# Kernel tuning notes

Hardware: AMD Instinct MI355X
Metric: run time of the kernel (lower is better)

The kernel has to match this reference:

```python
import jax, jax.numpy as jnp
import numpy as np
import math

B, L, D, H = 2, 2048, 1024, 16
DH = D // H
TAU = 1.0
EPS_LN = 1e-12


def neural_sort(scores, tau=TAU):
    # scores: (B, n) -> soft permutation P_hat: (B, n, n)
    s = scores[..., None]                                   # (B,n,1)
    A = jnp.abs(s - jnp.swapaxes(s, 1, 2))                  # (B,n,n) pairwise |s_i - s_j|
    Bsum = jnp.sum(A, axis=-1, keepdims=True)               # row sums == A @ ones(n,n) columns
    n = scores.shape[-1]
    scaling = (n + 1 - 2 * (jnp.arange(n) + 1)).astype(scores.dtype)  # (n,)
    C = s * scaling[None, None, :]                          # (B,n,n)
    P_max = jnp.swapaxes(C - Bsum, 1, 2)
    return jax.nn.softmax(P_max / tau, axis=-1)


def euler_transform(v, delta, b_euler, log_scale, is_query):
    # v: (B,L,D); soft-sort channels, polar decompose, rotate, recompose
    Bv, Lv, Dv = v.shape
    scores = v.mean(axis=1)                                 # (B,D)
    P = neural_sort(scores)                                 # (B,D,D)
    v_sorted = jnp.einsum('bij,blj->bli', P, v)             # permute channel dim
    r, p = v_sorted[..., ::2], v_sorted[..., 1::2]          # (B,L,D/2)
    lam = jnp.sqrt(r * r + p * p + 1e-6)
    lam_d = jax.lax.stop_gradient(lam)
    theta = jnp.arctan2(p / lam_d, r / lam_d)
    theta = theta * delta
    if is_query:
        theta = theta + b_euler
    lam = lam * jnp.exp(jnp.clip(log_scale, -5.0, 5.0))
    out = jnp.stack([lam * jnp.cos(theta), lam * jnp.sin(theta)], axis=-1)
    return out.reshape(Bv, Lv, Dv)


def layer_norm(x, gamma, beta, eps=EPS_LN):
    mu = x.mean(axis=-1, keepdims=True)
    var = ((x - mu) ** 2).mean(axis=-1, keepdims=True)
    return (x - mu) / jnp.sqrt(var + eps) * gamma + beta


def forward(input_tensor, Wq, bq, Wk, bk, Wv, bv, Wd, bd, gamma, beta, delta, b_euler, log_scale):
    q = input_tensor @ Wq.T + bq
    k = input_tensor @ Wk.T + bk
    v = input_tensor @ Wv.T + bv
    q = euler_transform(q, delta, b_euler, log_scale, is_query=True)
    k = euler_transform(k, delta, b_euler, log_scale, is_query=False)
    def heads(x):
        return x.reshape(B, L, H, DH).transpose(0, 2, 1, 3)  # (B,H,L,DH)
    qh, kh, vh = heads(q), heads(k), heads(v)
    scores = jnp.einsum('bhqd,bhkd->bhqk', qh, kh) / math.sqrt(DH)
    probs = jax.nn.softmax(scores, axis=-1)                 # dropout off (eval)
    ctx = jnp.einsum('bhqk,bhkd->bhqd', probs, vh)
    ctx = ctx.transpose(0, 2, 1, 3).reshape(B, L, D)
    hidden = ctx @ Wd.T + bd
    return layer_norm(hidden + input_tensor, gamma, beta)


def setup_inputs() -> dict:
    key = jax.random.key(0)
    ks = jax.random.split(key, 16)
    s = 1.0 / math.sqrt(D)
    return {
        'input_tensor': jax.random.normal(ks[0], (B, L, D), jnp.float32),
        'Wq': jax.random.normal(ks[1], (D, D), jnp.float32) * s,
        'bq': jnp.zeros((D,), jnp.float32),
        'Wk': jax.random.normal(ks[2], (D, D), jnp.float32) * s,
        'bk': jnp.zeros((D,), jnp.float32),
        'Wv': jax.random.normal(ks[3], (D, D), jnp.float32) * s,
        'bv': jnp.zeros((D,), jnp.float32),
        'Wd': jax.random.normal(ks[4], (D, D), jnp.float32) * s,
        'bd': jnp.zeros((D,), jnp.float32),
        'gamma': jnp.ones((D,), jnp.float32),
        'beta': jnp.zeros((D,), jnp.float32),
        'delta': jnp.full((1, 1, D // 2), 0.1, jnp.float32),
        'b_euler': jnp.zeros((1, 1, D // 2), jnp.float32),
        'log_scale': jnp.zeros((1, 1, D // 2), jnp.float32),
    }


def reference(input_tensor, Wq, bq, Wk, bk, Wv, bv, Wd, bd, gamma, beta, delta, b_euler, log_scale):
    return forward(input_tensor, Wq, bq, Wk, bk, Wv, bv, Wd, bd, gamma, beta, delta, b_euler, log_scale)
```

## Files before the change

kernel.cpp:

```cpp
#include <hip/hip_runtime.h>


typedef unsigned short bf16_t;
typedef short frag_ab __attribute__((ext_vector_type(8)));
typedef float frag_cd __attribute__((ext_vector_type(4)));

#define BB 2
#define LL 2048
#define DD 1024
#define HH 16
#define DH 64

__device__ __forceinline__ float b2f(bf16_t u) {
  union { unsigned int i; float f; } c; c.i = ((unsigned int)u) << 16; return c.f;
}
__device__ __forceinline__ bf16_t f2b(float f) {
  union { float f; unsigned int i; } c; c.f = f;
  unsigned int r = c.i + 0x7fffu + ((c.i >> 16) & 1u);
  return (bf16_t)(r >> 16);
}
__device__ __forceinline__ unsigned int fbits(float f) {
  union { float f; unsigned int i; } c; c.f = f; return c.i;
}
__device__ __forceinline__ float waveMax(float v) {
#pragma unroll
  for (int m = 32; m > 0; m >>= 1) v = fmaxf(v, __shfl_xor(v, m));
  return v;
}
__device__ __forceinline__ float waveSum(float v) {
#pragma unroll
  for (int m = 32; m > 0; m >>= 1) v += __shfl_xor(v, m);
  return v;
}

__device__ __forceinline__ void gll16(const bf16_t* g, bf16_t* l) {
  __builtin_amdgcn_global_load_lds(
      (const __attribute__((address_space(1))) void*)g,
      (__attribute__((address_space(3))) void*)l, 16, 0, 0);
}

__global__ __launch_bounds__(256) void cast_f2b(const float* __restrict__ in,
                                                bf16_t* __restrict__ out, int n4) {
  const int i = blockIdx.x * 256 + threadIdx.x;
  if (i < n4) {
    float4 v = ((const float4*)in)[i];
    ushort4 o;
    o.x = f2b(v.x); o.y = f2b(v.y); o.z = f2b(v.z); o.w = f2b(v.w);
    ((ushort4*)out)[i] = o;
  }
}

__global__ __launch_bounds__(256) void cast_wvd(const float* __restrict__ Wv,
                                                const float* __restrict__ Wd,
                                                bf16_t* __restrict__ Wvb,
                                                bf16_t* __restrict__ Wdb) {
  const float* in = blockIdx.z ? Wd : Wv;
  bf16_t* out = blockIdx.z ? Wdb : Wvb;
  const int i = blockIdx.x * 256 + threadIdx.x;
  float4 v = ((const float4*)in)[i];
  ushort4 o;
  o.x = f2b(v.x); o.y = f2b(v.y); o.z = f2b(v.z); o.w = f2b(v.w);
  ((ushort4*)out)[i] = o;
}

__global__ __launch_bounds__(256) void cast_transpose_w(const float* __restrict__ Wq,
                                                        const float* __restrict__ Wk,
                                                        bf16_t* __restrict__ WqT,
                                                        bf16_t* __restrict__ WkT) {
  const float* W = blockIdx.z ? Wk : Wq;
  bf16_t* WT = blockIdx.z ? WkT : WqT;
  __shared__ bf16_t T[64][72];
  const int i0 = blockIdx.x * 64, m0 = blockIdx.y * 64;
  const int tid = threadIdx.x;
#pragma unroll
  for (int it = 0; it < 4; ++it) {
    const int idx = tid + it * 256;
    const int r = idx >> 4, c4 = (idx & 15) * 4;
    float4 v = *(const float4*)&W[(size_t)(i0 + r) * DD + m0 + c4];
    T[c4 + 0][r] = f2b(v.x);
    T[c4 + 1][r] = f2b(v.y);
    T[c4 + 2][r] = f2b(v.z);
    T[c4 + 3][r] = f2b(v.w);
  }
  __syncthreads();
#pragma unroll
  for (int it = 0; it < 2; ++it) {
    const int idx = tid + it * 256;
    const int r = idx >> 3, seg = idx & 7;
    *(uint4*)&WT[(size_t)(m0 + r) * DD + i0 + seg * 8] = *(const uint4*)&T[r][seg * 8];
  }
}

struct GemmB { const bf16_t* A; const bf16_t* Bm; const float* bias; float* Cf; bf16_t* Cb; };
struct GemmArgs { GemmB gb[6]; };

__global__ __launch_bounds__(256) void gemm128(GemmArgs ga, int M, int N, int K) {
  const GemmB g = ga.gb[blockIdx.z];
  const int bm = blockIdx.y * 128, bn = blockIdx.x * 128;
  __shared__ bf16_t As[128][32];
  __shared__ bf16_t Bs[128][32];
  bf16_t* As_f = &As[0][0];
  bf16_t* Bs_f = &Bs[0][0];
  const int tid = threadIdx.x;
  const int lane = tid & 63, w = tid >> 6;
  const int quad = lane >> 4, l16 = lane & 15;
  const int wm = (w >> 1) * 64, wn = (w & 1) * 64;
  const int wbase = w << 9;

  frag_cd acc[4][4];
#pragma unroll
  for (int i = 0; i < 4; ++i)
#pragma unroll
    for (int j = 0; j < 4; ++j)
#pragma unroll
      for (int r = 0; r < 4; ++r) acc[i][j][r] = 0.f;

  const int r0 = tid >> 2, s0 = (tid & 3) * 8;
  const int r1 = (tid + 256) >> 2, s1 = ((tid + 256) & 3) * 8;
  const size_t aoff0 = (size_t)(bm + r0) * K + s0;
  const size_t aoff1 = (size_t)(bm + r1) * K + s1;
  const size_t boff0 = (size_t)(bn + r0) * K + s0;
  const size_t boff1 = (size_t)(bn + r1) * K + s1;

  for (int k0 = 0; k0 < K; k0 += 32) {
    __syncthreads();
    gll16(g.A + aoff0 + k0, As_f + wbase);
    gll16(g.A + aoff1 + k0, As_f + 2048 + wbase);
    gll16(g.Bm + boff0 + k0, Bs_f + wbase);
    gll16(g.Bm + boff1 + k0, Bs_f + 2048 + wbase);
    __syncthreads();
    frag_ab af[4], bfr[4];
#pragma unroll
    for (int i = 0; i < 4; ++i) {
      af[i]  = *(const frag_ab*)&As[wm + i * 16 + l16][quad * 8];
      bfr[i] = *(const frag_ab*)&Bs[wn + i * 16 + l16][quad * 8];
    }
#pragma unroll
    for (int i = 0; i < 4; ++i)
#pragma unroll
      for (int j = 0; j < 4; ++j)
        acc[i][j] = __builtin_amdgcn_mfma_f32_16x16x32_bf16(af[i], bfr[j], acc[i][j], 0, 0, 0);
  }

#pragma unroll
  for (int i = 0; i < 4; ++i) {
#pragma unroll
    for (int r = 0; r < 4; ++r) {
      const int row = bm + wm + i * 16 + quad * 4 + r;
#pragma unroll
      for (int j = 0; j < 4; ++j) {
        const int col = bn + wn + j * 16 + l16;
        float v = acc[i][j][r];
        if (g.bias) v += g.bias[col];
        if (g.Cf) g.Cf[(size_t)row * N + col] = v;
        if (g.Cb) g.Cb[(size_t)row * N + col] = f2b(v);
      }
    }
  }
}

__global__ __launch_bounds__(256) void gemm64(GemmArgs ga, int M, int N, int K) {
  const GemmB g = ga.gb[blockIdx.z];
  const int bm = blockIdx.y * 64, bn = blockIdx.x * 128;
  __shared__ bf16_t As[64][32];
  __shared__ bf16_t Bs[128][32];
  bf16_t* As_f = &As[0][0];
  bf16_t* Bs_f = &Bs[0][0];
  const int tid = threadIdx.x;
  const int lane = tid & 63, w = tid >> 6;
  const int quad = lane >> 4, l16 = lane & 15;
  const int wm = (w >> 1) * 32, wn = (w & 1) * 64;
  const int wbase = w << 9;

  frag_cd acc[2][4];
#pragma unroll
  for (int i = 0; i < 2; ++i)
#pragma unroll
    for (int j = 0; j < 4; ++j)
#pragma unroll
      for (int r = 0; r < 4; ++r) acc[i][j][r] = 0.f;

  const int r0 = tid >> 2, s0 = (tid & 3) * 8;
  const int r1 = (tid + 256) >> 2, s1 = ((tid + 256) & 3) * 8;
  const size_t aoff0 = (size_t)(bm + r0) * K + s0;
  const size_t boff0 = (size_t)(bn + r0) * K + s0;
  const size_t boff1 = (size_t)(bn + r1) * K + s1;

  for (int k0 = 0; k0 < K; k0 += 32) {
    __syncthreads();
    gll16(g.A + aoff0 + k0, As_f + wbase);
    gll16(g.Bm + boff0 + k0, Bs_f + wbase);
    gll16(g.Bm + boff1 + k0, Bs_f + 2048 + wbase);
    __syncthreads();
    frag_ab af[2], bfr[4];
#pragma unroll
    for (int i = 0; i < 2; ++i)
      af[i] = *(const frag_ab*)&As[wm + i * 16 + l16][quad * 8];
#pragma unroll
    for (int j = 0; j < 4; ++j)
      bfr[j] = *(const frag_ab*)&Bs[wn + j * 16 + l16][quad * 8];
#pragma unroll
    for (int i = 0; i < 2; ++i)
#pragma unroll
      for (int j = 0; j < 4; ++j)
        acc[i][j] = __builtin_amdgcn_mfma_f32_16x16x32_bf16(af[i], bfr[j], acc[i][j], 0, 0, 0);
  }

#pragma unroll
  for (int i = 0; i < 2; ++i) {
#pragma unroll
    for (int r = 0; r < 4; ++r) {
      const int row = bm + wm + i * 16 + quad * 4 + r;
#pragma unroll
      for (int j = 0; j < 4; ++j) {
        const int col = bn + wn + j * 16 + l16;
        float v = acc[i][j][r];
        if (g.bias) v += g.bias[col];
        if (g.Cf) g.Cf[(size_t)row * N + col] = v;
        if (g.Cb) g.Cb[(size_t)row * N + col] = f2b(v);
      }
    }
  }
}

__global__ __launch_bounds__(256) void xmean_kernel(const float* __restrict__ X,
                                                    float* __restrict__ xmean) {
  const int d = blockIdx.x * 256 + threadIdx.x;
  const int b = blockIdx.z;
  const int l0 = blockIdx.y * 64;
  float s = 0.f;
  for (int l = l0; l < l0 + 64; ++l)
    s += X[((size_t)b * LL + l) * DD + d];
  atomicAdd(&xmean[b * DD + d], s * (1.f / (float)LL));
}

__global__ __launch_bounds__(256) void scores_gemm(const float* __restrict__ xmean,
                                                   const float* __restrict__ Wq,
                                                   const float* __restrict__ bq,
                                                   const float* __restrict__ Wk,
                                                   const float* __restrict__ bk,
                                                   float* __restrict__ scores) {
  const int w = threadIdx.x >> 6, lane = threadIdx.x & 63;
  const int idx = blockIdx.x * 4 + w;
  const int t = idx >> 11, b = (idx >> 10) & 1, i = idx & 1023;
  const float* W = t ? Wk : Wq;
  const float* bias = t ? bk : bq;
  const float* xm = xmean + b * DD;
  float sum = 0.f;
#pragma unroll
  for (int k = 0; k < 4; ++k) {
    float4 wv = *(const float4*)&W[(size_t)i * DD + k * 256 + lane * 4];
    float4 xv = *(const float4*)&xm[k * 256 + lane * 4];
    sum += wv.x * xv.x + wv.y * xv.y + wv.z * xv.z + wv.w * xv.w;
  }
  sum = waveSum(sum);
  if (lane == 0) scores[idx] = sum + bias[i];
}

__global__ __launch_bounds__(256) void bsum_kernel(const float* __restrict__ scores,
                                                   float* __restrict__ bsum) {
  __shared__ float sc[DD];
  const int z = blockIdx.x, jb = blockIdx.y, tid = threadIdx.x;
#pragma unroll
  for (int s = 0; s < 4; ++s) sc[tid + s * 256] = scores[z * DD + tid + s * 256];
  __syncthreads();
  const int j = jb * 256 + tid;
  const float si = sc[j];
  float s = 0.f;
  for (int m = 0; m < DD; m += 4) {
    float4 v = *(const float4*)&sc[m];
    s += fabsf(si - v.x) + fabsf(si - v.y) + fabsf(si - v.z) + fabsf(si - v.w);
  }
  bsum[z * DD + j] = s;
}

__global__ __launch_bounds__(256) void p_kernel(const float* __restrict__ scores,
                                                const float* __restrict__ bsum,
                                                const float* __restrict__ bq,
                                                const float* __restrict__ bk,
                                                bf16_t* __restrict__ Pq,
                                                bf16_t* __restrict__ Pk,
                                                float* __restrict__ bias4) {
  const int i = blockIdx.x;
  const int z = blockIdx.y;
  const int t = z >> 1, b = z & 1;
  const float* sc = scores + z * DD;
  const float* bs = bsum + z * DD;
  const float* bias = t ? bk : bq;
  const float scal = 1023.f - 2.f * (float)i;
  const int tid = threadIdx.x;
  __shared__ float redA[4], redB[4], redC[4];

  float lg[4], bb[4];
  float mx = -1e30f;
#pragma unroll
  for (int s = 0; s < 4; ++s) {
    const int j = tid + s * 256;
    lg[s] = sc[j] * scal - bs[j];
    bb[s] = bias[j];
    mx = fmaxf(mx, lg[s]);
  }
  mx = waveMax(mx);
  if ((tid & 63) == 0) redA[tid >> 6] = mx;
  __syncthreads();
  const float M = fmaxf(fmaxf(redA[0], redA[1]), fmaxf(redA[2], redA[3]));
  float sum = 0.f, dot = 0.f;
#pragma unroll
  for (int s = 0; s < 4; ++s) {
    lg[s] = __expf(lg[s] - M);
    sum += lg[s];
    dot += lg[s] * bb[s];
  }
  sum = waveSum(sum); dot = waveSum(dot);
  if ((tid & 63) == 0) { redB[tid >> 6] = sum; redC[tid >> 6] = dot; }
  __syncthreads();
  const float inv = 1.f / (redB[0] + redB[1] + redB[2] + redB[3]);
  bf16_t* P = (t ? Pk : Pq) + ((size_t)b << 20) + (size_t)i * DD;
#pragma unroll
  for (int s = 0; s < 4; ++s) P[tid + s * 256] = f2b(lg[s] * inv);
  if (tid == 0)
    bias4[t * 2048 + b * 1024 + i] = (redC[0] + redC[1] + redC[2] + redC[3]) * inv;
}

__global__ __launch_bounds__(256) void euler_kernel(bf16_t* __restrict__ qs,
                                                    bf16_t* __restrict__ ks,
                                                    const float* __restrict__ delta,
                                                    const float* __restrict__ beul,
                                                    const float* __restrict__ lsc) {
  const int isq = (blockIdx.y == 0);
  unsigned int* buf = (unsigned int*)(isq ? qs : ks);
  const int idx = blockIdx.x * 256 + threadIdx.x;
  const int c = idx & 511;
  const size_t n = idx >> 9;
  const unsigned int u = buf[n * 512 + c];
  const float r = b2f((bf16_t)(u & 0xffffu));
  const float p = b2f((bf16_t)(u >> 16));
  float lam = sqrtf(r * r + p * p + 1e-6f);
  float th = atan2f(p, r) * delta[c];
  if (isq) th += beul[c];
  lam *= __expf(fminf(fmaxf(lsc[c], -5.f), 5.f));
  float sn, cs;
  __sincosf(th, &sn, &cs);
  buf[n * 512 + c] = ((unsigned int)f2b(lam * sn) << 16) | (unsigned int)f2b(lam * cs);
}

__global__ __launch_bounds__(256) void transpose_v(const bf16_t* __restrict__ vb,
                                                   bf16_t* __restrict__ vbT) {
  __shared__ bf16_t T[64][72];
  const int l0 = blockIdx.x * 64, d0 = blockIdx.y * 64, b = blockIdx.z;
  const int tid = threadIdx.x;
  for (int i = tid; i < 512; i += 256) {
    const int r = i >> 3, seg = i & 7;
    uint4 v = *(const uint4*)&vb[((size_t)b * LL + l0 + r) * DD + d0 + seg * 8];
    const bf16_t* vs = (const bf16_t*)&v;
#pragma unroll
    for (int j = 0; j < 8; ++j) T[seg * 8 + j][r] = vs[j];
  }
  __syncthreads();
  for (int i = tid; i < 512; i += 256) {
    const int r = i >> 3, seg = i & 7;
    *(uint4*)&vbT[((size_t)b * DD + d0 + r) * LL + l0 + seg * 8] =
        *(const uint4*)&T[r][seg * 8];
  }
}

__global__ __launch_bounds__(256) void attn_kernel(const bf16_t* __restrict__ Q,
                                                   const bf16_t* __restrict__ Kt,
                                                   const bf16_t* __restrict__ VT,
                                                   bf16_t* __restrict__ O) {
  const int bid = blockIdx.x;
  const int g = (bid & 7) + 8 * (bid >> 8);
  const int qt = (bid >> 3) & 31;
  const int b = g >> 4, h = g & 15;
  const int q0 = qt * 64;
  const int tid = threadIdx.x, w = tid >> 6, lane = tid & 63;
  const int quad = lane >> 4, l16 = lane & 15;
  __shared__ bf16_t Ks[64][72], Vs[64][72], Ps[64][72], Qs[64][72];
  const size_t base = ((size_t)b * LL) * DD + (size_t)h * DH;
  const size_t vtb = (size_t)(b * DD + h * DH) * LL;

  for (int i = tid; i < 512; i += 256) {
    const int r = i >> 3, seg = i & 7;
    *(uint4*)&Qs[r][seg * 8] = *(const uint4*)&Q[base + (size_t)(q0 + r) * DD + seg * 8];
  }
  __syncthreads();
  frag_ab bq0 = *(const frag_ab*)&Qs[w * 16 + l16][quad * 8];
  frag_ab bq1 = *(const frag_ab*)&Qs[w * 16 + l16][32 + quad * 8];

  float lsum = 0.f;
  frag_cd o_[4];
#pragma unroll
  for (int n = 0; n < 4; ++n)
#pragma unroll
    for (int r = 0; r < 4; ++r) o_[n][r] = 0.f;

  for (int kt = 0; kt < LL / 64; ++kt) {
    __syncthreads();
    for (int i = tid; i < 512; i += 256) {
      const int r = i >> 3, seg = i & 7;
      *(uint4*)&Ks[r][seg * 8] = *(const uint4*)&Kt[base + (size_t)(kt * 64 + r) * DD + seg * 8];
      *(uint4*)&Vs[r][seg * 8] = *(const uint4*)&VT[vtb + (size_t)r * LL + kt * 64 + seg * 8];
    }
    __syncthreads();

#pragma unroll
    for (int n = 0; n < 4; ++n) {
      frag_ab ak0 = *(const frag_ab*)&Ks[n * 16 + l16][quad * 8];
      frag_ab ak1 = *(const frag_ab*)&Ks[n * 16 + l16][32 + quad * 8];
      frag_cd z; z[0] = z[1] = z[2] = z[3] = 0.f;
      z = __builtin_amdgcn_mfma_f32_16x16x32_bf16(ak0, bq0, z, 0, 0, 0);
      z = __builtin_amdgcn_mfma_f32_16x16x32_bf16(ak1, bq1, z, 0, 0, 0);
      float p0 = __expf(z[0] * 0.125f - 12.f);
      float p1 = __expf(z[1] * 0.125f - 12.f);
      float p2 = __expf(z[2] * 0.125f - 12.f);
      float p3 = __expf(z[3] * 0.125f - 12.f);
      lsum += p0 + p1 + p2 + p3;
      unsigned int u01 = __builtin_amdgcn_perm(fbits(p1), fbits(p0), 0x07060302u);
      unsigned int u23 = __builtin_amdgcn_perm(fbits(p3), fbits(p2), 0x07060302u);
      uint2 pk; pk.x = u01; pk.y = u23;
      *(uint2*)&Ps[w * 16 + l16][n * 16 + quad * 4] = pk;
    }

    frag_ab ap0 = *(const frag_ab*)&Ps[w * 16 + l16][quad * 8];
    frag_ab ap1 = *(const frag_ab*)&Ps[w * 16 + l16][32 + quad * 8];
#pragma unroll
    for (int n = 0; n < 4; ++n) {
      frag_ab bv0 = *(const frag_ab*)&Vs[n * 16 + l16][quad * 8];
      frag_ab bv1 = *(const frag_ab*)&Vs[n * 16 + l16][32 + quad * 8];
      o_[n] = __builtin_amdgcn_mfma_f32_16x16x32_bf16(ap0, bv0, o_[n], 0, 0, 0);
      o_[n] = __builtin_amdgcn_mfma_f32_16x16x32_bf16(ap1, bv1, o_[n], 0, 0, 0);
    }
  }

  lsum += __shfl_xor(lsum, 16);
  lsum += __shfl_xor(lsum, 32);
  float lfin[4];
#pragma unroll
  for (int r = 0; r < 4; ++r) lfin[r] = __shfl(lsum, quad * 4 + r);

#pragma unroll
  for (int n = 0; n < 4; ++n)
#pragma unroll
    for (int r = 0; r < 4; ++r) {
      const float v = o_[n][r] / lfin[r];
      O[base + (size_t)(q0 + w * 16 + quad * 4 + r) * DD + n * 16 + l16] = f2b(v);
    }
}

__global__ __launch_bounds__(256) void ln_kernel(const bf16_t* __restrict__ hidden,
                                                 const float* __restrict__ x0,
                                                 const float* __restrict__ gamma,
                                                 const float* __restrict__ beta,
                                                 float* __restrict__ out) {
  const int row = blockIdx.x;
  const int tid = threadIdx.x;
  __shared__ float red1[4], red2[4];
  float v[4];
  float s1 = 0.f, s2 = 0.f;
#pragma unroll
  for (int s = 0; s < 4; ++s) {
    const int c = tid + s * 256;
    const float x = b2f(hidden[(size_t)row * DD + c]) + x0[(size_t)row * DD + c];
    v[s] = x; s1 += x; s2 += x * x;
  }
  s1 = waveSum(s1); s2 = waveSum(s2);
  if ((tid & 63) == 0) { red1[tid >> 6] = s1; red2[tid >> 6] = s2; }
  __syncthreads();
  const float t1 = red1[0] + red1[1] + red1[2] + red1[3];
  const float t2 = red2[0] + red2[1] + red2[2] + red2[3];
  const float mu = t1 * (1.f / DD);
  const float var = t2 * (1.f / DD) - mu * mu;
  const float inv = rsqrtf(var + 1e-12f);
#pragma unroll
  for (int s = 0; s < 4; ++s) {
    const int c = tid + s * 256;
    out[(size_t)row * DD + c] = (v[s] - mu) * inv * gamma[c] + beta[c];
  }
}

extern "C" void kernel_launch(void* const* d_in, const int* in_sizes, int n_in,
                              void* d_out, int out_size, void* d_ws, size_t ws_size,
                              hipStream_t stream) {
  const float* X    = (const float*)d_in[0];
  const float* Wq   = (const float*)d_in[1];
  const float* bq   = (const float*)d_in[2];
  const float* Wk   = (const float*)d_in[3];
  const float* bk   = (const float*)d_in[4];
  const float* Wv   = (const float*)d_in[5];
  const float* bv   = (const float*)d_in[6];
  const float* Wd   = (const float*)d_in[7];
  const float* bd   = (const float*)d_in[8];
  const float* gam  = (const float*)d_in[9];
  const float* bet  = (const float*)d_in[10];
  const float* delt = (const float*)d_in[11];
  const float* beul = (const float*)d_in[12];
  const float* lsc  = (const float*)d_in[13];
  float* out = (float*)d_out;

  char* w = (char*)d_ws;
  const size_t MB = 1024ull * 1024ull;
  bf16_t* Xb  = (bf16_t*)(w + 0 * MB);
  bf16_t* Wvb = (bf16_t*)(w + 8 * MB);
  bf16_t* Wdb = (bf16_t*)(w + 10 * MB);
  bf16_t* WqT = (bf16_t*)(w + 12 * MB);
  bf16_t* WkT = (bf16_t*)(w + 14 * MB);
  bf16_t* Pq  = (bf16_t*)(w + 16 * MB);
  bf16_t* Pk  = (bf16_t*)(w + 20 * MB);
  bf16_t* Wp  = (bf16_t*)(w + 24 * MB);
  bf16_t* vb  = (bf16_t*)(w + 32 * MB);
  bf16_t* qs  = (bf16_t*)(w + 40 * MB);
  bf16_t* ks  = (bf16_t*)(w + 48 * MB);
  bf16_t* vbT = (bf16_t*)(w + 56 * MB);
  bf16_t* ctx = (bf16_t*)(w + 64 * MB);
  bf16_t* hid = (bf16_t*)(w + 24 * MB);
  float*  xmean  = (float*)(w + 72 * MB);
  float*  scores = (float*)(w + 72 * MB + 16384);
  float*  bsum   = (float*)(w + 72 * MB + 32768);
  float*  bias4  = (float*)(w + 72 * MB + 49152);

  const size_t WSZ = (size_t)DD * DD;

  cast_f2b<<<dim3(4096), 256, 0, stream>>>(X, Xb, BB * LL * DD / 4);
  cast_wvd<<<dim3(1024, 1, 2), 256, 0, stream>>>(Wv, Wd, Wvb, Wdb);
  cast_transpose_w<<<dim3(16, 16, 2), 256, 0, stream>>>(Wq, Wk, WqT, WkT);

  hipMemsetAsync(xmean, 0, BB * DD * sizeof(float), stream);
  xmean_kernel<<<dim3(4, 32, 2), 256, 0, stream>>>(X, xmean);
  scores_gemm<<<dim3(1024), 256, 0, stream>>>(xmean, Wq, bq, Wk, bk, scores);

  bsum_kernel<<<dim3(4, 4), 256, 0, stream>>>(scores, bsum);
  p_kernel<<<dim3(1024, 4), 256, 0, stream>>>(scores, bsum, bq, bk, Pq, Pk, bias4);

  GemmArgs gw = {};
  gw.gb[0] = {Pq,       WqT, nullptr, nullptr, Wp};
  gw.gb[1] = {Pq + WSZ, WqT, nullptr, nullptr, Wp + WSZ};
  gw.gb[2] = {Pk,       WkT, nullptr, nullptr, Wp + 2 * WSZ};
  gw.gb[3] = {Pk + WSZ, WkT, nullptr, nullptr, Wp + 3 * WSZ};
  gemm64<<<dim3(8, 16, 4), 256, 0, stream>>>(gw, DD, DD, DD);

  const size_t XHALF = (size_t)LL * DD;
  GemmArgs gs = {};
  gs.gb[0] = {Xb,         Wp,           bias4,        nullptr, qs};
  gs.gb[1] = {Xb + XHALF, Wp + WSZ,     bias4 + 1024, nullptr, qs + XHALF};
  gs.gb[2] = {Xb,         Wp + 2 * WSZ, bias4 + 2048, nullptr, ks};
  gs.gb[3] = {Xb + XHALF, Wp + 3 * WSZ, bias4 + 3072, nullptr, ks + XHALF};
  gs.gb[4] = {Xb,         Wvb,          bv,           nullptr, vb};
  gs.gb[5] = {Xb + XHALF, Wvb,          bv,           nullptr, vb + XHALF};
  gemm128<<<dim3(8, 16, 6), 256, 0, stream>>>(gs, LL, DD, DD);

  transpose_v<<<dim3(32, 16, 2), 256, 0, stream>>>(vb, vbT);
  euler_kernel<<<dim3(8192, 2), 256, 0, stream>>>(qs, ks, delt, beul, lsc);

  attn_kernel<<<dim3(1024), 256, 0, stream>>>(qs, ks, vbT, ctx);

  GemmArgs g4 = {};
  g4.gb[0] = {ctx, Wdb, bd, nullptr, hid};
  gemm64<<<dim3(8, 64, 1), 256, 0, stream>>>(g4, BB * LL, DD, DD);

  ln_kernel<<<dim3(BB * LL), 256, 0, stream>>>(hid, X, gam, bet, out);
}
```

Measured before the change: 320.3 us.

## Fuse prep and euler/transpose launches, shrink GEMM tiles, fold softmax scale into Q

Merges the input/weight casts and the xmean memset into one kernel, and the euler transform plus V transpose into another, which cuts launch count. The 64-row GEMM switches to 64x64 tiles so the grids have more blocks. Attention now folds the 1/sqrt(d)·log2e scale into Q, starts the MFMA accumulator at a constant offset, and uses exp2. The row sum comes from an extra MFMA against a ones row padded into V shared memory, replacing the shuffle reduction. These trade a little extra MFMA work and bf16 scaling of Q for fewer ALU ops and fewer launches.

```diff
diff --git a/kernel.cpp b/kernel.cpp
--- a/kernel.cpp
+++ b/kernel.cpp
@@ -11,6 +11,9 @@
 #define HH 16
 #define DH 64
 
+#define QSCALE 0.18033688f
+#define EOFF  -17.3123404907f
+
 __device__ __forceinline__ float b2f(bf16_t u) {
   union { unsigned int i; float f; } c; c.i = ((unsigned int)u) << 16; return c.f;
 }
@@ -39,24 +42,25 @@
       (__attribute__((address_space(3))) void*)l, 16, 0, 0);
 }
 
-__global__ __launch_bounds__(256) void cast_f2b(const float* __restrict__ in,
-                                                bf16_t* __restrict__ out, int n4) {
-  const int i = blockIdx.x * 256 + threadIdx.x;
-  if (i < n4) {
-    float4 v = ((const float4*)in)[i];
-    ushort4 o;
-    o.x = f2b(v.x); o.y = f2b(v.y); o.z = f2b(v.z); o.w = f2b(v.w);
-    ((ushort4*)out)[i] = o;
-  }
-}
-
-__global__ __launch_bounds__(256) void cast_wvd(const float* __restrict__ Wv,
-                                                const float* __restrict__ Wd,
-                                                bf16_t* __restrict__ Wvb,
-                                                bf16_t* __restrict__ Wdb) {
-  const float* in = blockIdx.z ? Wd : Wv;
-  bf16_t* out = blockIdx.z ? Wdb : Wvb;
-  const int i = blockIdx.x * 256 + threadIdx.x;
+__global__ __launch_bounds__(256) void prep_cast(const float* __restrict__ X,
+                                                 const float* __restrict__ Wv,
+                                                 const float* __restrict__ Wd,
+                                                 bf16_t* __restrict__ Xb,
+                                                 bf16_t* __restrict__ Wvb,
+                                                 bf16_t* __restrict__ Wdb,
+                                                 float* __restrict__ xmean) {
+  const int bid = blockIdx.x;
+  if (bid == 6144) {
+    if (threadIdx.x < 256)
+      for (int i = threadIdx.x; i < BB * DD; i += 256) xmean[i] = 0.f;
+    return;
+  }
+  const float* in;
+  bf16_t* out;
+  int i;
+  if (bid < 4096)      { in = X;  out = Xb;  i = bid * 256 + threadIdx.x; }
+  else if (bid < 5120) { in = Wv; out = Wvb; i = (bid - 4096) * 256 + threadIdx.x; }
+  else                 { in = Wd; out = Wdb; i = (bid - 5120) * 256 + threadIdx.x; }
   float4 v = ((const float4*)in)[i];
   ushort4 o;
   o.x = f2b(v.x); o.y = f2b(v.y); o.z = f2b(v.z); o.w = f2b(v.w);
@@ -159,50 +163,46 @@
   }
 }
 
-__global__ __launch_bounds__(256) void gemm64(GemmArgs ga, int M, int N, int K) {
+__global__ __launch_bounds__(256) void gemm64x64(GemmArgs ga, int M, int N, int K) {
   const GemmB g = ga.gb[blockIdx.z];
-  const int bm = blockIdx.y * 64, bn = blockIdx.x * 128;
+  const int bm = blockIdx.y * 64, bn = blockIdx.x * 64;
   __shared__ bf16_t As[64][32];
-  __shared__ bf16_t Bs[128][32];
+  __shared__ bf16_t Bs[64][32];
   bf16_t* As_f = &As[0][0];
   bf16_t* Bs_f = &Bs[0][0];
   const int tid = threadIdx.x;
   const int lane = tid & 63, w = tid >> 6;
   const int quad = lane >> 4, l16 = lane & 15;
-  const int wm = (w >> 1) * 32, wn = (w & 1) * 64;
+  const int wm = (w >> 1) * 32, wn = (w & 1) * 32;
   const int wbase = w << 9;
 
-  frag_cd acc[2][4];
+  frag_cd acc[2][2];
 #pragma unroll
   for (int i = 0; i < 2; ++i)
 #pragma unroll
-    for (int j = 0; j < 4; ++j)
+    for (int j = 0; j < 2; ++j)
 #pragma unroll
       for (int r = 0; r < 4; ++r) acc[i][j][r] = 0.f;
 
   const int r0 = tid >> 2, s0 = (tid & 3) * 8;
-  const int r1 = (tid + 256) >> 2, s1 = ((tid + 256) & 3) * 8;
   const size_t aoff0 = (size_t)(bm + r0) * K + s0;
   const size_t boff0 = (size_t)(bn + r0) * K + s0;
-  const size_t boff1 = (size_t)(bn + r1) * K + s1;
 
   for (int k0 = 0; k0 < K; k0 += 32) {
     __syncthreads();
     gll16(g.A + aoff0 + k0, As_f + wbase);
     gll16(g.Bm + boff0 + k0, Bs_f + wbase);
-    gll16(g.Bm + boff1 + k0, Bs_f + 2048 + wbase);
     __syncthreads();
-    frag_ab af[2], bfr[4];
+    frag_ab af[2], bfr[2];
+#pragma unroll
+    for (int i = 0; i < 2; ++i) {
+      af[i]  = *(const frag_ab*)&As[wm + i * 16 + l16][quad * 8];
+      bfr[i] = *(const frag_ab*)&Bs[wn + i * 16 + l16][quad * 8];
+    }
 #pragma unroll
     for (int i = 0; i < 2; ++i)
-      af[i] = *(const frag_ab*)&As[wm + i * 16 + l16][quad * 8];
-#pragma unroll
-    for (int j = 0; j < 4; ++j)
-      bfr[j] = *(const frag_ab*)&Bs[wn + j * 16 + l16][quad * 8];
-#pragma unroll
-    for (int i = 0; i < 2; ++i)
-#pragma unroll
-      for (int j = 0; j < 4; ++j)
+#pragma unroll
+      for (int j = 0; j < 2; ++j)
         acc[i][j] = __builtin_amdgcn_mfma_f32_16x16x32_bf16(af[i], bfr[j], acc[i][j], 0, 0, 0);
   }
 
@@ -212,7 +212,7 @@
     for (int r = 0; r < 4; ++r) {
       const int row = bm + wm + i * 16 + quad * 4 + r;
 #pragma unroll
-      for (int j = 0; j < 4; ++j) {
+      for (int j = 0; j < 2; ++j) {
         const int col = bn + wn + j * 16 + l16;
         float v = acc[i][j][r];
         if (g.bias) v += g.bias[col];
@@ -322,33 +322,37 @@
     bias4[t * 2048 + b * 1024 + i] = (redC[0] + redC[1] + redC[2] + redC[3]) * inv;
 }
 
-__global__ __launch_bounds__(256) void euler_kernel(bf16_t* __restrict__ qs,
+__global__ __launch_bounds__(256) void euler_transv(bf16_t* __restrict__ qs,
                                                     bf16_t* __restrict__ ks,
                                                     const float* __restrict__ delta,
                                                     const float* __restrict__ beul,
-                                                    const float* __restrict__ lsc) {
-  const int isq = (blockIdx.y == 0);
-  unsigned int* buf = (unsigned int*)(isq ? qs : ks);
-  const int idx = blockIdx.x * 256 + threadIdx.x;
-  const int c = idx & 511;
-  const size_t n = idx >> 9;
-  const unsigned int u = buf[n * 512 + c];
-  const float r = b2f((bf16_t)(u & 0xffffu));
-  const float p = b2f((bf16_t)(u >> 16));
-  float lam = sqrtf(r * r + p * p + 1e-6f);
-  float th = atan2f(p, r) * delta[c];
-  if (isq) th += beul[c];
-  lam *= __expf(fminf(fmaxf(lsc[c], -5.f), 5.f));
-  float sn, cs;
-  __sincosf(th, &sn, &cs);
-  buf[n * 512 + c] = ((unsigned int)f2b(lam * sn) << 16) | (unsigned int)f2b(lam * cs);
-}
-
-__global__ __launch_bounds__(256) void transpose_v(const bf16_t* __restrict__ vb,
-                                                   bf16_t* __restrict__ vbT) {
+                                                    const float* __restrict__ lsc,
+                                                    const bf16_t* __restrict__ vb,
+                                                    bf16_t* __restrict__ vbT) {
   __shared__ bf16_t T[64][72];
-  const int l0 = blockIdx.x * 64, d0 = blockIdx.y * 64, b = blockIdx.z;
+  const int bid = blockIdx.x;
   const int tid = threadIdx.x;
+  if (bid < 16384) {
+    const int isq = (bid < 8192);
+    unsigned int* buf = (unsigned int*)(isq ? qs : ks);
+    const int idx = (isq ? bid : bid - 8192) * 256 + tid;
+    const int c = idx & 511;
+    const size_t n = idx >> 9;
+    const unsigned int u = buf[n * 512 + c];
+    const float r = b2f((bf16_t)(u & 0xffffu));
+    const float p = b2f((bf16_t)(u >> 16));
+    float lam = sqrtf(r * r + p * p + 1e-6f);
+    float th = atan2f(p, r) * delta[c];
+    if (isq) th += beul[c];
+    lam *= __expf(fminf(fmaxf(lsc[c], -5.f), 5.f));
+    if (isq) lam *= QSCALE;
+    float sn, cs;
+    __sincosf(th, &sn, &cs);
+    buf[n * 512 + c] = ((unsigned int)f2b(lam * sn) << 16) | (unsigned int)f2b(lam * cs);
+    return;
+  }
+  const int tb = bid - 16384;
+  const int l0 = (tb & 31) * 64, d0 = ((tb >> 5) & 15) * 64, b = tb >> 9;
   for (int i = tid; i < 512; i += 256) {
     const int r = i >> 3, seg = i & 7;
     uint4 v = *(const uint4*)&vb[((size_t)b * LL + l0 + r) * DD + d0 + seg * 8];
@@ -375,10 +379,14 @@
   const int q0 = qt * 64;
   const int tid = threadIdx.x, w = tid >> 6, lane = tid & 63;
   const int quad = lane >> 4, l16 = lane & 15;
-  __shared__ bf16_t Ks[64][72], Vs[64][72], Ps[64][72], Qs[64][72];
+  __shared__ bf16_t Ks[64][72], Vs[80][72], Ps[64][72], Qs[64][72];
   const size_t base = ((size_t)b * LL) * DD + (size_t)h * DH;
   const size_t vtb = (size_t)(b * DD + h * DH) * LL;
 
+  for (int i = tid; i < 16 * 72; i += 256) {
+    const int r = i / 72;
+    Vs[64 + r][i % 72] = (r == 0) ? (bf16_t)0x3F80 : (bf16_t)0;
+  }
   for (int i = tid; i < 512; i += 256) {
     const int r = i >> 3, seg = i & 7;
     *(uint4*)&Qs[r][seg * 8] = *(const uint4*)&Q[base + (size_t)(q0 + r) * DD + seg * 8];
@@ -387,12 +395,13 @@
   frag_ab bq0 = *(const frag_ab*)&Qs[w * 16 + l16][quad * 8];
   frag_ab bq1 = *(const frag_ab*)&Qs[w * 16 + l16][32 + quad * 8];
 
-  float lsum = 0.f;
-  frag_cd o_[4];
+  frag_cd o_[4], l5;
 #pragma unroll
   for (int n = 0; n < 4; ++n)
 #pragma unroll
     for (int r = 0; r < 4; ++r) o_[n][r] = 0.f;
+#pragma unroll
+  for (int r = 0; r < 4; ++r) l5[r] = 0.f;
 
   for (int kt = 0; kt < LL / 64; ++kt) {
     __syncthreads();
@@ -407,14 +416,13 @@
     for (int n = 0; n < 4; ++n) {
       frag_ab ak0 = *(const frag_ab*)&Ks[n * 16 + l16][quad * 8];
       frag_ab ak1 = *(const frag_ab*)&Ks[n * 16 + l16][32 + quad * 8];
-      frag_cd z; z[0] = z[1] = z[2] = z[3] = 0.f;
+      frag_cd z; z[0] = z[1] = z[2] = z[3] = EOFF;
       z = __builtin_amdgcn_mfma_f32_16x16x32_bf16(ak0, bq0, z, 0, 0, 0);
       z = __builtin_amdgcn_mfma_f32_16x16x32_bf16(ak1, bq1, z, 0, 0, 0);
-      float p0 = __expf(z[0] * 0.125f - 12.f);
-      float p1 = __expf(z[1] * 0.125f - 12.f);
-      float p2 = __expf(z[2] * 0.125f - 12.f);
-      float p3 = __expf(z[3] * 0.125f - 12.f);
-      lsum += p0 + p1 + p2 + p3;
+      float p0 = __builtin_amdgcn_exp2f(z[0]);
+      float p1 = __builtin_amdgcn_exp2f(z[1]);
+      float p2 = __builtin_amdgcn_exp2f(z[2]);
+      float p3 = __builtin_amdgcn_exp2f(z[3]);
       unsigned int u01 = __builtin_amdgcn_perm(fbits(p1), fbits(p0), 0x07060302u);
       unsigned int u23 = __builtin_amdgcn_perm(fbits(p3), fbits(p2), 0x07060302u);
       uint2 pk; pk.x = u01; pk.y = u23;
@@ -430,19 +438,21 @@
       o_[n] = __builtin_amdgcn_mfma_f32_16x16x32_bf16(ap0, bv0, o_[n], 0, 0, 0);
       o_[n] = __builtin_amdgcn_mfma_f32_16x16x32_bf16(ap1, bv1, o_[n], 0, 0, 0);
     }
-  }
-
-  lsum += __shfl_xor(lsum, 16);
-  lsum += __shfl_xor(lsum, 32);
+    frag_ab bo0 = *(const frag_ab*)&Vs[64 + l16][quad * 8];
+    frag_ab bo1 = *(const frag_ab*)&Vs[64 + l16][32 + quad * 8];
+    l5 = __builtin_amdgcn_mfma_f32_16x16x32_bf16(ap0, bo0, l5, 0, 0, 0);
+    l5 = __builtin_amdgcn_mfma_f32_16x16x32_bf16(ap1, bo1, l5, 0, 0, 0);
+  }
+
   float lfin[4];
 #pragma unroll
-  for (int r = 0; r < 4; ++r) lfin[r] = __shfl(lsum, quad * 4 + r);
+  for (int r = 0; r < 4; ++r) lfin[r] = 1.f / __shfl(l5[r], quad << 4);
 
 #pragma unroll
   for (int n = 0; n < 4; ++n)
 #pragma unroll
     for (int r = 0; r < 4; ++r) {
-      const float v = o_[n][r] / lfin[r];
+      const float v = o_[n][r] * lfin[r];
       O[base + (size_t)(q0 + w * 16 + quad * 4 + r) * DD + n * 16 + l16] = f2b(v);
     }
 }
@@ -520,11 +530,9 @@
 
   const size_t WSZ = (size_t)DD * DD;
 
-  cast_f2b<<<dim3(4096), 256, 0, stream>>>(X, Xb, BB * LL * DD / 4);
-  cast_wvd<<<dim3(1024, 1, 2), 256, 0, stream>>>(Wv, Wd, Wvb, Wdb);
+  prep_cast<<<dim3(6145), 256, 0, stream>>>(X, Wv, Wd, Xb, Wvb, Wdb, xmean);
   cast_transpose_w<<<dim3(16, 16, 2), 256, 0, stream>>>(Wq, Wk, WqT, WkT);
 
-  hipMemsetAsync(xmean, 0, BB * DD * sizeof(float), stream);
   xmean_kernel<<<dim3(4, 32, 2), 256, 0, stream>>>(X, xmean);
   scores_gemm<<<dim3(1024), 256, 0, stream>>>(xmean, Wq, bq, Wk, bk, scores);
 
@@ -536,7 +544,7 @@
   gw.gb[1] = {Pq + WSZ, WqT, nullptr, nullptr, Wp + WSZ};
   gw.gb[2] = {Pk,       WkT, nullptr, nullptr, Wp + 2 * WSZ};
   gw.gb[3] = {Pk + WSZ, WkT, nullptr, nullptr, Wp + 3 * WSZ};
-  gemm64<<<dim3(8, 16, 4), 256, 0, stream>>>(gw, DD, DD, DD);
+  gemm64x64<<<dim3(16, 16, 4), 256, 0, stream>>>(gw, DD, DD, DD);
 
   const size_t XHALF = (size_t)LL * DD;
   GemmArgs gs = {};
@@ -548,14 +556,13 @@
   gs.gb[5] = {Xb + XHALF, Wvb,          bv,           nullptr, vb + XHALF};
   gemm128<<<dim3(8, 16, 6), 256, 0, stream>>>(gs, LL, DD, DD);
 
-  transpose_v<<<dim3(32, 16, 2), 256, 0, stream>>>(vb, vbT);
-  euler_kernel<<<dim3(8192, 2), 256, 0, stream>>>(qs, ks, delt, beul, lsc);
+  euler_transv<<<dim3(17408), 256, 0, stream>>>(qs, ks, delt, beul, lsc, vb, vbT);
 
   attn_kernel<<<dim3(1024), 256, 0, stream>>>(qs, ks, vbT, ctx);
 
   GemmArgs g4 = {};
   g4.gb[0] = {ctx, Wdb, bd, nullptr, hid};
-  gemm64<<<dim3(8, 64, 1), 256, 0, stream>>>(g4, BB * LL, DD, DD);
+  gemm64x64<<<dim3(16, 64, 1), 256, 0, stream>>>(g4, BB * LL, DD, DD);
 
   ln_kernel<<<dim3(BB * LL), 256, 0, stream>>>(hid, X, gam, bet, out);
 }
```

After: 309.3 us. -3.5%, faster.
